# Kernel tuning notes

Hardware: AMD Instinct MI355X
Metric: run time of the kernel (lower is better)

## Reference

```python
import jax, jax.numpy as jnp
import numpy as np

D_MODEL = 1024
N_HEADS = 16
D_HEAD = D_MODEL // N_HEADS


def setup_inputs() -> dict:
    key = jax.random.key(0)
    k1, k2, k3 = jax.random.split(key, 3)
    B, T = 2, 2048
    x = jax.random.normal(k1, (B, T, D_MODEL), dtype=jnp.float32)
    # Linear weights stored as (in, out), equivalent to torch W^T
    w_qkv = jax.random.normal(k2, (D_MODEL, 3 * D_MODEL), dtype=jnp.float32) * (D_MODEL ** -0.5)
    w_proj = jax.random.normal(k3, (D_MODEL, D_MODEL), dtype=jnp.float32) * (D_MODEL ** -0.5)
    return {"x": x, "w_qkv": w_qkv, "w_proj": w_proj}


def reference(x, w_qkv, w_proj):
    B, T, C = x.shape
    qkv = x @ w_qkv                                   # (B, T, 3C)
    qkv = qkv.reshape(B, T, 3, N_HEADS, D_HEAD)
    q, k, v = qkv[:, :, 0], qkv[:, :, 1], qkv[:, :, 2]  # (B, T, H, dh)
    q = q.transpose(0, 2, 1, 3)                        # (B, H, T, dh)
    k = k.transpose(0, 2, 1, 3)
    v = v.transpose(0, 2, 1, 3)
    scale = 1.0 / jnp.sqrt(jnp.float32(D_HEAD))
    scores = jnp.einsum('bhqd,bhkd->bhqk', q, k) * scale  # (B, H, T, T)
    causal = jnp.tril(jnp.ones((T, T), dtype=bool))
    scores = jnp.where(causal, scores, jnp.float32(-jnp.inf))
    w = jax.nn.softmax(scores, axis=-1)
    ctx = jnp.einsum('bhqk,bhkd->bhqd', w, v)          # (B, H, T, dh)
    ctx = ctx.transpose(0, 2, 1, 3).reshape(B, T, C)
    return ctx @ w_proj
```

## Files before the change

kernel.cpp:

```cpp
#include <hip/hip_runtime.h>
#include <hip/hip_bf16.h>
#include <math.h>
#include <stdint.h>

#define D_MODEL 1024
#define NHEADS  16
#define DHEAD   64
#define BATCH   2
#define SEQ     2048
#define ROWS    (BATCH*SEQ)

#define NEG_BIG (-1e30f)
#define QSCALE  0.18033688011112042f

typedef __bf16 bf16v8 __attribute__((ext_vector_type(8)));
typedef short  shortv8 __attribute__((ext_vector_type(8)));
typedef short  shortv4 __attribute__((ext_vector_type(4)));
typedef float  floatv4 __attribute__((ext_vector_type(4)));
typedef unsigned short ush;

__device__ __forceinline__ ush f2b(float f) {
  return __builtin_bit_cast(ush, (__bf16)f);
}

__device__ __forceinline__ void async16(ush* lds, const ush* g) {
  __builtin_amdgcn_global_load_lds(
      (const __attribute__((address_space(1))) void*)g,
      (__attribute__((address_space(3))) void*)lds, 16, 0, 0);
}

__global__ __launch_bounds__(256)
void prep(const uint32_t* __restrict__ x, ush* __restrict__ xb,
          const void* __restrict__ wqkv, ush* __restrict__ wqkvT,
          const void* __restrict__ wproj, ush* __restrict__ wprojT,
          int* __restrict__ flagp) {
  __shared__ int sflag;
  __shared__ __align__(16) ush tile[64][72];

  int bid = blockIdx.x;
  int t   = threadIdx.x;

  if (t < 64) {
    uint32_t e = (x[t] >> 7) & 0xFF;
    unsigned long long m = __ballot(e >= 96 && e <= 144);
    if (t == 0) sflag = (__popcll(m) >= 32) ? 1 : 0;
  }
  __syncthreads();
  int isbf = sflag;
  if (bid == 0 && t == 0) *flagp = isbf;

  if (bid < 2048) {
    size_t i = (size_t)bid * 256 + t;
    if (isbf) {
      ((shortv8*)xb)[i] = ((const shortv8*)x)[i];
    } else {
      const floatv4* p = ((const floatv4*)x) + i * 2;
      floatv4 a = p[0], b = p[1];
      shortv8 o;
#pragma unroll
      for (int j = 0; j < 4; ++j) { o[j] = (short)f2b(a[j]); o[4+j] = (short)f2b(b[j]); }
      ((shortv8*)xb)[i] = o;
    }
  } else {
    const void* W; ush* Wt; int N, b2;
    const int K = 1024;
    if (bid < 2816) { W = wqkv;  Wt = wqkvT;  N = 3072; b2 = bid - 2048; }
    else            { W = wproj; Wt = wprojT; N = 1024; b2 = bid - 2816; }
    int tiles_n = N >> 6;
    int tk = b2 / tiles_n;
    int tn = b2 % tiles_n;
    int r  = t >> 2;
    int c8 = (t & 3) * 8;

    if (isbf) {
      const ush* src = (const ush*)W + (size_t)(tk*64 + r) * N + tn*64;
#pragma unroll
      for (int c = 0; c < 2; ++c)
        *(shortv8*)&tile[r][c8 + c*32] = *(const shortv8*)&src[c8 + c*32];
    } else {
      const float* src = (const float*)W + (size_t)(tk*64 + r) * N + tn*64;
#pragma unroll
      for (int c = 0; c < 2; ++c) {
        const floatv4* p = (const floatv4*)&src[c8 + c*32];
        floatv4 a = p[0], b = p[1];
        shortv8 o;
#pragma unroll
        for (int j = 0; j < 4; ++j) { o[j] = (short)f2b(a[j]); o[4+j] = (short)f2b(b[j]); }
        *(shortv8*)&tile[r][c8 + c*32] = o;
      }
    }
    __syncthreads();
    ush* dst = Wt + (size_t)(tn*64 + r) * K + tk*64;
#pragma unroll
    for (int c = 0; c < 2; ++c) {
      int k8 = c8 + c*32;
      shortv8 v;
#pragma unroll
      for (int j = 0; j < 8; ++j) v[j] = (short)tile[k8 + j][r];
      *(shortv8*)&dst[k8] = v;
    }
  }
}

#define GEMM_PROLOG(Aq, Bq)                                                 \
  __shared__ __align__(16) ush smem[16384];                                 \
  const int K = 1024;                                                       \
  int bid = blockIdx.x;                                                     \
  int m0 = (bid / tiles_n) * 128;                                           \
  int n0 = (bid % tiles_n) * 128;                                           \
  int t    = threadIdx.x;                                                   \
  int lane = t & 63;                                                        \
  int w    = t >> 6;                                                        \
  int wm   = (w >> 1) * 64;                                                 \
  int wn   = (w & 1) * 64;                                                  \
  int lr   = lane & 15;                                                     \
  int quad = lane >> 4;                                                     \
  floatv4 acc[4][4] = {};                                                   \
  int r16 = lane >> 2;                                                      \
  int g4  = (lane & 3) ^ (r16 & 3);                                         \
  const ush* gA0 = Aq + (size_t)(m0 + 32*w + r16)*K + g4*8;                 \
  const ush* gA1 = gA0 + (size_t)16*K;                                      \
  const ush* gB0 = Bq + (size_t)(n0 + 32*w + r16)*K + g4*8;                 \
  const ush* gB1 = gB0 + (size_t)16*K;                                      \
  int fs = (quad ^ (lr & 3)) * 8;                                           \
  async16(&smem[(32*w)*32], gA0);                                           \
  async16(&smem[(32*w+16)*32], gA1);                                        \
  async16(&smem[8192 + (32*w)*32], gB0);                                    \
  async16(&smem[8192 + (32*w+16)*32], gB1);                                 \
  for (int kk = 0; kk < K; kk += 32) {                                      \
    int cur = (kk >> 5) & 1;                                                \
    __syncthreads();                                                        \
    if (kk + 32 < K) {                                                      \
      int nx = cur ^ 1;                                                     \
      async16(&smem[nx*4096 + (32*w)*32], gA0 + kk + 32);                   \
      async16(&smem[nx*4096 + (32*w+16)*32], gA1 + kk + 32);                \
      async16(&smem[8192 + nx*4096 + (32*w)*32], gB0 + kk + 32);            \
      async16(&smem[8192 + nx*4096 + (32*w+16)*32], gB1 + kk + 32);         \
    }                                                                       \
    bf16v8 af[4], bfr[4];                                                   \
    _Pragma("unroll")                                                       \
    for (int i = 0; i < 4; ++i) {                                           \
      af[i]  = *(bf16v8*)&smem[cur*4096 + (wm + i*16 + lr)*32 + fs];        \
      bfr[i] = *(bf16v8*)&smem[8192 + cur*4096 + (wn + i*16 + lr)*32 + fs]; \
    }                                                                       \
    _Pragma("unroll")                                                       \
    for (int i = 0; i < 4; ++i)                                             \
      _Pragma("unroll")                                                     \
      for (int j = 0; j < 4; ++j)                                           \
        acc[i][j] = __builtin_amdgcn_mfma_f32_16x16x32_bf16(bfr[i], af[j],  \
                                                            acc[i][j], 0, 0, 0); \
  }

__global__ __launch_bounds__(256, 3)
void gemm_qkv(const ush* __restrict__ A, const ush* __restrict__ Bt,
              ush* __restrict__ qb_, ush* __restrict__ kb_, ush* __restrict__ vb_,
              int tiles_n) {
  GEMM_PROLOG(A, Bt)

  int nwb = n0 + wn;
  int s   = nwb >> 10;
  int h   = (nwb & 1023) >> 6;
  int b   = (m0 + wm) >> 11;
  int bh  = b*16 + h;
  int ttw = (m0 + wm) & 2047;

  __syncthreads();

  if (s < 2) {
    ush* dst = (s == 0) ? qb_ : kb_;
    float sc = (s == 0) ? QSCALE : 1.0f;
#pragma unroll
    for (int i = 0; i < 4; ++i) {
      int d4 = i*16 + quad*4;
#pragma unroll
      for (int j = 0; j < 4; ++j) {
        int tt = ttw + j*16 + lr;
        shortv4 v4;
#pragma unroll
        for (int r = 0; r < 4; ++r) v4[r] = (short)f2b(acc[i][j][r] * sc);
        *(shortv4*)&dst[((size_t)bh*SEQ + tt)*64 + d4] = v4;
      }
    }
  } else {
    ush* L = &smem[w*4096];
#pragma unroll
    for (int i = 0; i < 4; ++i) {
#pragma unroll
      for (int r = 0; r < 4; ++r) {
        int dl = i*16 + quad*4 + r;
        shortv4 p4;
#pragma unroll
        for (int j = 0; j < 4; ++j) p4[j] = (short)f2b(acc[i][j][r]);
        int slot = (lr >> 1) ^ (dl & 7);
        *(shortv4*)&L[dl*64 + slot*8 + (lr & 1)*4] = p4;
      }
    }
#pragma unroll
    for (int p = 0; p < 8; ++p) {
      int dl = p*8 + (lane >> 3);
      int c8 = lane & 7;
      int slot = c8 ^ (dl & 7);
      shortv8 v = *(shortv8*)&L[dl*64 + slot*8];
      *(shortv8*)&vb_[((size_t)bh*64 + dl)*SEQ + ttw + c8*8] = v;
    }
  }
}

__global__ __launch_bounds__(256, 4)
void gemm_bt(const ush* __restrict__ A, const ush* __restrict__ Bt,
             void* __restrict__ Cp, const int* __restrict__ flag,
             int ldc, int tiles_n) {
  __shared__ __align__(16) ush smem[12288];
  const int K = 1024;
  int bid = blockIdx.x;
  int m0 = (bid / tiles_n) * 64;
  int n0 = (bid % tiles_n) * 128;
  int t    = threadIdx.x;
  int lane = t & 63;
  int w    = t >> 6;
  int wm   = (w >> 1) * 32;
  int wn   = (w & 1) * 64;
  int lr   = lane & 15;
  int quad = lane >> 4;
  floatv4 acc[4][2] = {};
  int r16 = lane >> 2;
  int g4  = (lane & 3) ^ (r16 & 3);
  const ush* gA0 = A  + (size_t)(m0 + 16*w + r16)*K + g4*8;
  const ush* gB0 = Bt + (size_t)(n0 + 32*w + r16)*K + g4*8;
  const ush* gB1 = gB0 + (size_t)16*K;
  int fs = (quad ^ (lr & 3)) * 8;

  async16(&smem[(16*w)*32], gA0);
  async16(&smem[4096 + (32*w)*32], gB0);
  async16(&smem[4096 + (32*w+16)*32], gB1);

  for (int kk = 0; kk < K; kk += 32) {
    int cur = (kk >> 5) & 1;
    __syncthreads();
    if (kk + 32 < K) {
      int nx = cur ^ 1;
      async16(&smem[nx*2048 + (16*w)*32], gA0 + kk + 32);
      async16(&smem[4096 + nx*4096 + (32*w)*32], gB0 + kk + 32);
      async16(&smem[4096 + nx*4096 + (32*w+16)*32], gB1 + kk + 32);
    }
    bf16v8 af[2], bfr[4];
#pragma unroll
    for (int j = 0; j < 2; ++j)
      af[j] = *(bf16v8*)&smem[cur*2048 + (wm + j*16 + lr)*32 + fs];
#pragma unroll
    for (int i = 0; i < 4; ++i)
      bfr[i] = *(bf16v8*)&smem[4096 + cur*4096 + (wn + i*16 + lr)*32 + fs];
#pragma unroll
    for (int i = 0; i < 4; ++i)
#pragma unroll
      for (int j = 0; j < 2; ++j)
        acc[i][j] = __builtin_amdgcn_mfma_f32_16x16x32_bf16(bfr[i], af[j],
                                                            acc[i][j], 0, 0, 0);
  }

  int f32out = (flag != nullptr) && (*flag == 0);
  if (f32out) {
    float* Cf = (float*)Cp;
#pragma unroll
    for (int i = 0; i < 4; ++i) {
      int nb = n0 + wn + i*16 + quad*4;
#pragma unroll
      for (int j = 0; j < 2; ++j) {
        int row = m0 + wm + j*16 + lr;
        *(floatv4*)&Cf[(size_t)row*ldc + nb] = acc[i][j];
      }
    }
  } else {
    __hip_bfloat16* Cb = (__hip_bfloat16*)Cp;
#pragma unroll
    for (int i = 0; i < 4; ++i) {
      int nb = n0 + wn + i*16 + quad*4;
#pragma unroll
      for (int j = 0; j < 2; ++j) {
        int row = m0 + wm + j*16 + lr;
        shortv4 v4;
#pragma unroll
        for (int r = 0; r < 4; ++r) v4[r] = (short)f2b(acc[i][j][r]);
        *(shortv4*)&((ush*)Cb)[(size_t)row*ldc + nb] = v4;
      }
    }
  }
}

#define PSTR 72
#define MFMA16(a,b,c) __builtin_amdgcn_mfma_f32_16x16x32_bf16(a,b,c,0,0,0)

__device__ __forceinline__ void softpack(const floatv4* s, int qw, int kb0,
                                         bool diag, ush* PsW, int quad, int lr) {
  if (diag) {
#pragma unroll
    for (int r = 0; r < 4; ++r) {
      int qv = qw + quad*4 + r;
      shortv4 p4;
#pragma unroll
      for (int j = 0; j < 4; ++j) {
        float z = (kb0 + 16*j + lr > qv) ? NEG_BIG : s[j][r];
        p4[j] = (short)f2b(__builtin_amdgcn_exp2f(z));
      }
      *(shortv4*)&PsW[(quad*4 + r)*PSTR + lr*4] = p4;
    }
  } else {
#pragma unroll
    for (int r = 0; r < 4; ++r) {
      shortv4 p4;
#pragma unroll
      for (int j = 0; j < 4; ++j)
        p4[j] = (short)f2b(__builtin_amdgcn_exp2f(s[j][r]));
      *(shortv4*)&PsW[(quad*4 + r)*PSTR + lr*4] = p4;
    }
  }
}

__global__ __launch_bounds__(512, 4)
void attn_fwd(const ush* __restrict__ qb_, const ush* __restrict__ kb_,
              const ush* __restrict__ vb_, __hip_bfloat16* __restrict__ ctx) {
  __shared__ __align__(16) ush Ks[2][64*64];
  __shared__ __align__(16) ush Vt[2][64*64];
  __shared__ __align__(16) ush Ps[8][16*PSTR];

  int bid = blockIdx.x;
  int p   = bid & 15;
  int h   = (bid >> 4) & 15;
  int b   = bid >> 8;
  int bh  = b*16 + h;

  int t = threadIdx.x, w8 = t >> 6, lane = t & 63, lr = lane & 15, quad = lane >> 4;
  int isB = w8 >> 2;
  int w   = w8 & 3;

  const ush* qh = qb_ + (size_t)bh * SEQ * 64;
  const ush* kh = kb_ + (size_t)bh * SEQ * 64;
  const ush* vh = vb_ + (size_t)bh * 64 * SEQ;

  int qt = isB ? (31 - p) : p;
  int qw = qt*64 + w*16;

  const ush* qp = qh + (size_t)(qw + lr)*64;
  bf16v8 qf0 = *(const bf16v8*)&qp[quad*8];
  bf16v8 qf1 = *(const bf16v8*)&qp[32 + quad*8];

  floatv4 acc[4] = {}, acl = {};

  bf16v8 ones;
#pragma unroll
  for (int j = 0; j < 8; ++j) ones[j] = (__bf16)1.0f;

  int r8 = lane >> 3;
  int s8 = lane & 7;
  int g8 = s8 ^ r8;
  const ush* kg = kh + (size_t)(8*w8 + r8)*64 + g8*8;
  const ush* vg = vh + (size_t)(8*w8 + r8)*SEQ + g8*8;
  int lo = (8*w8)*64;

  int sl0 = quad ^ (lr & 7);
  int sl1 = (quad + 4) ^ (lr & 7);

  int ntiles = 32 - p;

  async16(&Ks[0][lo], kg);
  async16(&Vt[0][lo], vg);

  for (int tk = 0; tk < ntiles; ++tk) {
    int cur = tk & 1;
    __syncthreads();
    if (tk + 1 < ntiles) {
      int nx = cur ^ 1;
      async16(&Ks[nx][lo], kg + (size_t)(tk + 1) * 64 * 64);
      async16(&Vt[nx][lo], vg + (size_t)(tk + 1) * 64);
    }

    bool live = isB | (tk <= p);
    if (live) {
      int kb0 = tk * 64;
      bool diag = (tk == qt);

      floatv4 s[4] = {};
      __builtin_amdgcn_s_setprio(1);
#pragma unroll
      for (int j = 0; j < 4; ++j) {
        if (!diag || j <= w) {
          int row = 16*j + lr;
          bf16v8 kf0 = *(bf16v8*)&Ks[cur][row*64 + sl0*8];
          bf16v8 kf1 = *(bf16v8*)&Ks[cur][row*64 + sl1*8];
          s[j] = MFMA16(qf0, kf0, s[j]);
          s[j] = MFMA16(qf1, kf1, s[j]);
        }
      }
      __builtin_amdgcn_s_setprio(0);

      softpack(s, qw, kb0, diag, &Ps[w8][0], quad, lr);

      bf16v8 pf0 = *(bf16v8*)&Ps[w8][lr*PSTR + quad*8];
      bf16v8 pf1 = *(bf16v8*)&Ps[w8][lr*PSTR + 32 + quad*8];

      __builtin_amdgcn_s_setprio(1);
      acl = MFMA16(pf0, ones, acl);
      acl = MFMA16(pf1, ones, acl);

#pragma unroll
      for (int c = 0; c < 4; ++c) {
        int row = 16*c + lr;
        bf16v8 vf0 = *(bf16v8*)&Vt[cur][row*64 + sl0*8];
        bf16v8 vf1 = *(bf16v8*)&Vt[cur][row*64 + sl1*8];
        acc[c] = MFMA16(pf0, vf0, acc[c]);
        acc[c] = MFMA16(pf1, vf1, acc[c]);
      }
      __builtin_amdgcn_s_setprio(0);
    }
  }

#pragma unroll
  for (int r = 0; r < 4; ++r) {
    float inv = 1.0f / fmaxf(acl[r], 1e-30f);
    size_t o = (size_t)(b*SEQ + qw + quad*4 + r) * D_MODEL + h*64;
#pragma unroll
    for (int c = 0; c < 4; ++c)
      ctx[o + c*16 + lr] = __float2bfloat16(acc[c][r] * inv);
  }
}

extern "C" void kernel_launch(void* const* d_in, const int* in_sizes, int n_in,
                              void* d_out, int out_size, void* d_ws, size_t ws_size,
                              hipStream_t stream) {
  const void* x      = d_in[0];
  const void* w_qkv  = d_in[1];
  const void* w_proj = d_in[2];

  int* flag   = (int*)d_ws;
  ush* xb     = (ush*)d_ws + 8;
  ush* wqkvT  = xb     + (size_t)ROWS * D_MODEL;
  ush* wprojT = wqkvT  + (size_t)3072 * 1024;
  ush* qbuf   = wprojT + (size_t)1024 * 1024;
  ush* kbuf   = qbuf   + (size_t)32 * SEQ * 64;
  ush* vbuf   = kbuf   + (size_t)32 * SEQ * 64;
  ush* ctx    = xb;

  prep<<<3072, 256, 0, stream>>>((const uint32_t*)x, xb,
                                 w_qkv, wqkvT, w_proj, wprojT, flag);

  gemm_qkv<<<(ROWS/128)*(3072/128), 256, 0, stream>>>(
      xb, wqkvT, qbuf, kbuf, vbuf, 3072/128);

  attn_fwd<<<BATCH * NHEADS * 16, 512, 0, stream>>>(
      qbuf, kbuf, vbuf, (__hip_bfloat16*)ctx);

  gemm_bt<<<(ROWS/64)*(1024/128), 256, 0, stream>>>(
      ctx, wprojT, d_out, flag, 1024, 1024/128);
}
```

Before: 190.2 us.

## Rewrite QKV GEMM with 256x256 tiles, 8 waves and staggered async pipeline

Replaces the 128x128, 4-wave QKV projection GEMM with a 256x256 tile computed by 8 waves, each owning a 128x64 output region. The main loop uses K-steps of 64 with double-buffered LDS and splits the global loads into four quarter-tile groups that are interleaved with MFMA batches under partial vmcnt waits and raised wave priority. The goal is more data reuse per LDS byte and better overlap of loads with matrix math. The cost is 128KB of LDS per block, larger accumulator register pressure, and only 192 blocks, which may underfill the GPU's compute units.

```diff
diff --git a/kernel.cpp b/kernel.cpp
--- a/kernel.cpp
+++ b/kernel.cpp
@@ -102,106 +102,193 @@
   }
 }
 
-#define GEMM_PROLOG(Aq, Bq)                                                 \
-  __shared__ __align__(16) ush smem[16384];                                 \
-  const int K = 1024;                                                       \
-  int bid = blockIdx.x;                                                     \
-  int m0 = (bid / tiles_n) * 128;                                           \
-  int n0 = (bid % tiles_n) * 128;                                           \
-  int t    = threadIdx.x;                                                   \
-  int lane = t & 63;                                                        \
-  int w    = t >> 6;                                                        \
-  int wm   = (w >> 1) * 64;                                                 \
-  int wn   = (w & 1) * 64;                                                  \
-  int lr   = lane & 15;                                                     \
-  int quad = lane >> 4;                                                     \
-  floatv4 acc[4][4] = {};                                                   \
-  int r16 = lane >> 2;                                                      \
-  int g4  = (lane & 3) ^ (r16 & 3);                                         \
-  const ush* gA0 = Aq + (size_t)(m0 + 32*w + r16)*K + g4*8;                 \
-  const ush* gA1 = gA0 + (size_t)16*K;                                      \
-  const ush* gB0 = Bq + (size_t)(n0 + 32*w + r16)*K + g4*8;                 \
-  const ush* gB1 = gB0 + (size_t)16*K;                                      \
-  int fs = (quad ^ (lr & 3)) * 8;                                           \
-  async16(&smem[(32*w)*32], gA0);                                           \
-  async16(&smem[(32*w+16)*32], gA1);                                        \
-  async16(&smem[8192 + (32*w)*32], gB0);                                    \
-  async16(&smem[8192 + (32*w+16)*32], gB1);                                 \
-  for (int kk = 0; kk < K; kk += 32) {                                      \
-    int cur = (kk >> 5) & 1;                                                \
-    __syncthreads();                                                        \
-    if (kk + 32 < K) {                                                      \
-      int nx = cur ^ 1;                                                     \
-      async16(&smem[nx*4096 + (32*w)*32], gA0 + kk + 32);                   \
-      async16(&smem[nx*4096 + (32*w+16)*32], gA1 + kk + 32);                \
-      async16(&smem[8192 + nx*4096 + (32*w)*32], gB0 + kk + 32);            \
-      async16(&smem[8192 + nx*4096 + (32*w+16)*32], gB1 + kk + 32);         \
-    }                                                                       \
-    bf16v8 af[4], bfr[4];                                                   \
-    _Pragma("unroll")                                                       \
-    for (int i = 0; i < 4; ++i) {                                           \
-      af[i]  = *(bf16v8*)&smem[cur*4096 + (wm + i*16 + lr)*32 + fs];        \
-      bfr[i] = *(bf16v8*)&smem[8192 + cur*4096 + (wn + i*16 + lr)*32 + fs]; \
-    }                                                                       \
-    _Pragma("unroll")                                                       \
-    for (int i = 0; i < 4; ++i)                                             \
-      _Pragma("unroll")                                                     \
-      for (int j = 0; j < 4; ++j)                                           \
-        acc[i][j] = __builtin_amdgcn_mfma_f32_16x16x32_bf16(bfr[i], af[j],  \
-                                                            acc[i][j], 0, 0, 0); \
-  }
-
-__global__ __launch_bounds__(256, 3)
+#define MFMA16(a,b,c) __builtin_amdgcn_mfma_f32_16x16x32_bf16(a,b,c,0,0,0)
+
+__global__ __launch_bounds__(512, 2)
 void gemm_qkv(const ush* __restrict__ A, const ush* __restrict__ Bt,
-              ush* __restrict__ qb_, ush* __restrict__ kb_, ush* __restrict__ vb_,
-              int tiles_n) {
-  GEMM_PROLOG(A, Bt)
-
-  int nwb = n0 + wn;
-  int s   = nwb >> 10;
-  int h   = (nwb & 1023) >> 6;
-  int b   = (m0 + wm) >> 11;
+              ush* __restrict__ qb_, ush* __restrict__ kb_, ush* __restrict__ vb_) {
+  __shared__ __align__(16) ush smem[65536];
+  const int K = 1024;
+  const int tiles_n = 12;
+  int bid = blockIdx.x;
+  int m0 = (bid / tiles_n) * 256;
+  int n0 = (bid % tiles_n) * 256;
+  int t    = threadIdx.x;
+  int lane = t & 63;
+  int w    = t >> 6;
+  int wr   = w >> 2;
+  int wc   = w & 3;
+  int lr   = lane & 15;
+  int quad = lane >> 4;
+  int r8   = lane >> 3;
+  int s8   = lane & 7;
+  int g8   = s8 ^ r8;
+
+  int aeo = 2*w + (w>>2)*8;
+  int alo = aeo + 8;
+  int beo = (w>>1)*8 + (w&1)*2;
+  int blo = beo + 4;
+
+  const ush* gAe0 = A  + (size_t)(m0 + aeo*8     + r8)*K + g8*8;
+  const ush* gAe1 = gAe0 + (size_t)8*K;
+  const ush* gAl0 = A  + (size_t)(m0 + alo*8     + r8)*K + g8*8;
+  const ush* gAl1 = gAl0 + (size_t)8*K;
+  const ush* gBe0 = Bt + (size_t)(n0 + beo*8     + r8)*K + g8*8;
+  const ush* gBe1 = gBe0 + (size_t)8*K;
+  const ush* gBl0 = Bt + (size_t)(n0 + blo*8     + r8)*K + g8*8;
+  const ush* gBl1 = gBl0 + (size_t)8*K;
+
+  int lAe0 = aeo*512,         lAe1 = lAe0 + 512;
+  int lAl0 = alo*512,         lAl1 = lAl0 + 512;
+  int lBe0 = 32768 + beo*512, lBe1 = lBe0 + 512;
+  int lBl0 = 32768 + blo*512, lBl1 = lBl0 + 512;
+
+  floatv4 acc[4][8] = {};
+  bf16v8 af[4][2];
+  bf16v8 bf[4][2];
+
+  int sk0 = ((quad    ) ^ (lr & 7)) * 8;
+  int sk1 = ((quad + 4) ^ (lr & 7)) * 8;
+
+  async16(&smem[lAe0], gAe0); async16(&smem[lAe1], gAe1);
+  async16(&smem[lBe0], gBe0); async16(&smem[lBe1], gBe1);
+  async16(&smem[lBl0], gBl0); async16(&smem[lBl1], gBl1);
+  async16(&smem[lAl0], gAl0); async16(&smem[lAl1], gAl1);
+
+  for (int kt = 0; kt < 16; ++kt) {
+    int cur = kt & 1, nx = cur ^ 1;
+    int kn  = (kt + 1 < 16) ? (kt + 1) : 15;
+    int ko  = kn * 64;
+    int nb  = nx * 16384;
+
+    const ush* Ab = &smem[cur*16384 + (wr*128 + lr)*64];
+    const ush* Bb = &smem[32768 + cur*16384 + (wc*64 + lr)*64];
+
+    asm volatile("s_waitcnt vmcnt(4)" ::: "memory");
+    __builtin_amdgcn_s_barrier();
+
+#pragma unroll
+    for (int mi = 0; mi < 4; ++mi) {
+      af[mi][0] = *(const bf16v8*)&Ab[mi*1024 + sk0];
+      af[mi][1] = *(const bf16v8*)&Ab[mi*1024 + sk1];
+    }
+#pragma unroll
+    for (int ni = 0; ni < 2; ++ni) {
+      bf[ni][0] = *(const bf16v8*)&Bb[ni*1024 + sk0];
+      bf[ni][1] = *(const bf16v8*)&Bb[ni*1024 + sk1];
+    }
+    async16(&smem[nb + lAe0], gAe0 + ko); async16(&smem[nb + lAe1], gAe1 + ko);
+    __builtin_amdgcn_s_setprio(1);
+#pragma unroll
+    for (int ni = 0; ni < 2; ++ni)
+#pragma unroll
+      for (int mi = 0; mi < 4; ++mi)
+#pragma unroll
+        for (int ks = 0; ks < 2; ++ks)
+          acc[ni][mi] = MFMA16(bf[ni][ks], af[mi][ks], acc[ni][mi]);
+    __builtin_amdgcn_s_setprio(0);
+
+    asm volatile("s_waitcnt vmcnt(4)" ::: "memory");
+    __builtin_amdgcn_s_barrier();
+
+#pragma unroll
+    for (int ni = 0; ni < 2; ++ni) {
+      bf[2+ni][0] = *(const bf16v8*)&Bb[(2+ni)*1024 + sk0];
+      bf[2+ni][1] = *(const bf16v8*)&Bb[(2+ni)*1024 + sk1];
+    }
+    async16(&smem[nb + lBe0], gBe0 + ko); async16(&smem[nb + lBe1], gBe1 + ko);
+    __builtin_amdgcn_s_setprio(1);
+#pragma unroll
+    for (int ni = 0; ni < 2; ++ni)
+#pragma unroll
+      for (int mi = 0; mi < 4; ++mi)
+#pragma unroll
+        for (int ks = 0; ks < 2; ++ks)
+          acc[2+ni][mi] = MFMA16(bf[2+ni][ks], af[mi][ks], acc[2+ni][mi]);
+    __builtin_amdgcn_s_setprio(0);
+
+    asm volatile("s_waitcnt vmcnt(4)" ::: "memory");
+    __builtin_amdgcn_s_barrier();
+
+#pragma unroll
+    for (int mi = 0; mi < 4; ++mi) {
+      af[mi][0] = *(const bf16v8*)&Ab[4096 + mi*1024 + sk0];
+      af[mi][1] = *(const bf16v8*)&Ab[4096 + mi*1024 + sk1];
+    }
+    async16(&smem[nb + lBl0], gBl0 + ko); async16(&smem[nb + lBl1], gBl1 + ko);
+    __builtin_amdgcn_s_setprio(1);
+#pragma unroll
+    for (int ni = 0; ni < 2; ++ni)
+#pragma unroll
+      for (int mi = 0; mi < 4; ++mi)
+#pragma unroll
+        for (int ks = 0; ks < 2; ++ks)
+          acc[ni][4+mi] = MFMA16(bf[ni][ks], af[mi][ks], acc[ni][4+mi]);
+    __builtin_amdgcn_s_setprio(0);
+
+    __builtin_amdgcn_s_barrier();
+
+    async16(&smem[nb + lAl0], gAl0 + ko); async16(&smem[nb + lAl1], gAl1 + ko);
+    __builtin_amdgcn_s_setprio(1);
+#pragma unroll
+    for (int ni = 0; ni < 2; ++ni)
+#pragma unroll
+      for (int mi = 0; mi < 4; ++mi)
+#pragma unroll
+        for (int ks = 0; ks < 2; ++ks)
+          acc[2+ni][4+mi] = MFMA16(bf[2+ni][ks], af[mi][ks], acc[2+ni][4+mi]);
+    __builtin_amdgcn_s_setprio(0);
+  }
+
+  asm volatile("s_waitcnt vmcnt(0)" ::: "memory");
+  __builtin_amdgcn_s_barrier();
+
+  int s   = n0 >> 10;
+  int h   = ((n0 & 1023) + wc*64) >> 6;
+  int b   = (m0 + wr*128) >> 11;
   int bh  = b*16 + h;
-  int ttw = (m0 + wm) & 2047;
-
-  __syncthreads();
+  int ttw = (m0 + wr*128) & 2047;
 
   if (s < 2) {
     ush* dst = (s == 0) ? qb_ : kb_;
     float sc = (s == 0) ? QSCALE : 1.0f;
 #pragma unroll
-    for (int i = 0; i < 4; ++i) {
-      int d4 = i*16 + quad*4;
-#pragma unroll
-      for (int j = 0; j < 4; ++j) {
-        int tt = ttw + j*16 + lr;
+    for (int ni = 0; ni < 4; ++ni) {
+      int d4 = ni*16 + quad*4;
+#pragma unroll
+      for (int mi = 0; mi < 8; ++mi) {
+        int tt = ttw + mi*16 + lr;
         shortv4 v4;
 #pragma unroll
-        for (int r = 0; r < 4; ++r) v4[r] = (short)f2b(acc[i][j][r] * sc);
+        for (int r = 0; r < 4; ++r) v4[r] = (short)f2b(acc[ni][mi][r] * sc);
         *(shortv4*)&dst[((size_t)bh*SEQ + tt)*64 + d4] = v4;
       }
     }
   } else {
     ush* L = &smem[w*4096];
 #pragma unroll
-    for (int i = 0; i < 4; ++i) {
-#pragma unroll
-      for (int r = 0; r < 4; ++r) {
-        int dl = i*16 + quad*4 + r;
-        shortv4 p4;
-#pragma unroll
-        for (int j = 0; j < 4; ++j) p4[j] = (short)f2b(acc[i][j][r]);
-        int slot = (lr >> 1) ^ (dl & 7);
-        *(shortv4*)&L[dl*64 + slot*8 + (lr & 1)*4] = p4;
-      }
-    }
-#pragma unroll
-    for (int p = 0; p < 8; ++p) {
-      int dl = p*8 + (lane >> 3);
-      int c8 = lane & 7;
-      int slot = c8 ^ (dl & 7);
-      shortv8 v = *(shortv8*)&L[dl*64 + slot*8];
-      *(shortv8*)&vb_[((size_t)bh*64 + dl)*SEQ + ttw + c8*8] = v;
+    for (int th = 0; th < 2; ++th) {
+      int tw = ttw + th*64;
+#pragma unroll
+      for (int ni = 0; ni < 4; ++ni) {
+#pragma unroll
+        for (int r = 0; r < 4; ++r) {
+          int dl = ni*16 + quad*4 + r;
+          shortv4 p4;
+#pragma unroll
+          for (int j = 0; j < 4; ++j) p4[j] = (short)f2b(acc[ni][th*4 + j][r]);
+          int slot = (lr >> 1) ^ (dl & 7);
+          *(shortv4*)&L[dl*64 + slot*8 + (lr & 1)*4] = p4;
+        }
+      }
+#pragma unroll
+      for (int p = 0; p < 8; ++p) {
+        int dl = p*8 + (lane >> 3);
+        int c8 = lane & 7;
+        int slot = c8 ^ (dl & 7);
+        shortv8 v = *(shortv8*)&L[dl*64 + slot*8];
+        *(shortv8*)&vb_[((size_t)bh*64 + dl)*SEQ + tw + c8*8] = v;
+      }
     }
   }
 }
@@ -288,7 +375,6 @@
 }
 
 #define PSTR 72
-#define MFMA16(a,b,c) __builtin_amdgcn_mfma_f32_16x16x32_bf16(a,b,c,0,0,0)
 
 __device__ __forceinline__ void softpack(const floatv4* s, int qw, int kb0,
                                          bool diag, ush* PsW, int quad, int lr) {
@@ -443,8 +529,7 @@
   prep<<<3072, 256, 0, stream>>>((const uint32_t*)x, xb,
                                  w_qkv, wqkvT, w_proj, wprojT, flag);
 
-  gemm_qkv<<<(ROWS/128)*(3072/128), 256, 0, stream>>>(
-      xb, wqkvT, qbuf, kbuf, vbuf, 3072/128);
+  gemm_qkv<<<192, 512, 0, stream>>>(xb, wqkvT, qbuf, kbuf, vbuf);
 
   attn_fwd<<<BATCH * NHEADS * 16, 512, 0, stream>>>(
       qbuf, kbuf, vbuf, (__hip_bfloat16*)ctx);
```

New measurement: 178.5 us. -6.2%, faster.
